# Kernel optimization log

Measured on AMD Instinct MI355X. Metric: run time of the kernel, lower is better.

## Reference

```python
import jax, jax.numpy as jnp
import numpy as np

DIM_V = 512
NUM_HEADS = 8
LN_EPS = 1e-5


def _layernorm(x):
    # LayerNorm over last dim, no affine (simplified_layer_norm=True)
    mu = jnp.mean(x, axis=-1, keepdims=True)
    var = jnp.mean(jnp.square(x - mu), axis=-1, keepdims=True)
    return (x - mu) * jax.lax.rsqrt(var + LN_EPS)


def setup_inputs() -> dict:
    key = jax.random.key(0)
    ks = jax.random.split(key, 12)
    B, Nq, Nk, dQ, dK, dV = 16, 1024, 1024, 512, 512, DIM_V
    s = 0.02
    return {
        "Q": jax.random.normal(ks[0], (B, Nq, dQ), jnp.float32),
        "K": jax.random.normal(ks[1], (B, Nk, dK), jnp.float32),
        "Wq": jax.random.normal(ks[2], (dQ, dV), jnp.float32) * s,
        "bq": jnp.zeros((dV,), jnp.float32),
        "Wk": jax.random.normal(ks[3], (dK, dV), jnp.float32) * s,
        "bk": jnp.zeros((dV,), jnp.float32),
        "Wv": jax.random.normal(ks[4], (dK, dV), jnp.float32) * s,
        "bv": jnp.zeros((dV,), jnp.float32),
        "Wo": jax.random.normal(ks[5], (dV, dV), jnp.float32) * s,
        "bo": jnp.zeros((dV,), jnp.float32),
    }


def reference(Q, K, Wq, bq, Wk, bk, Wv, bv, Wo, bo):
    H = NUM_HEADS
    dh = DIM_V // H
    q = Q @ Wq + bq            # [B, Nq, dV]
    k = K @ Wk + bk            # [B, Nk, dV]
    v = K @ Wv + bv            # [B, Nk, dV]
    B, Nq, _ = q.shape
    Nk = k.shape[1]
    qh = q.reshape(B, Nq, H, dh)
    kh = k.reshape(B, Nk, H, dh)
    vh = v.reshape(B, Nk, H, dh)
    # NOTE: faithful to source — scale by sqrt(dim_V), not sqrt(head_dim)
    scores = jnp.einsum('bqhd,bkhd->bhqk', qh, kh) / jnp.sqrt(jnp.asarray(DIM_V, q.dtype))
    A = jax.nn.softmax(scores, axis=-1)                    # [B, H, Nq, Nk]
    attn = jnp.einsum('bhqk,bkhd->bqhd', A, vh).reshape(B, Nq, DIM_V)
    O = q + attn               # residual with projected Q
    O = _layernorm(O)          # ln0 (no affine)
    O = O + jax.nn.gelu(O @ Wo + bo, approximate=False)
    O = _layernorm(O)          # ln1 (no affine)
    return O
```

## Files before the change

kernel.cpp:

```cpp
#include <hip/hip_runtime.h>
#include <hip/hip_bf16.h>
#include <math.h>

typedef __bf16 bf16;
typedef __bf16 bf16x8 __attribute__((ext_vector_type(8)));
typedef __bf16 bf16x4 __attribute__((ext_vector_type(4)));
typedef float  f32x4  __attribute__((ext_vector_type(4)));

#define MFMA16(a,b,c) __builtin_amdgcn_mfma_f32_16x16x32_bf16((a),(b),(c),0,0,0)
#define ATT_SCALE 0.0441941738241592f

__device__ __forceinline__ void async16(const bf16* g, bf16* l) {
    __builtin_amdgcn_global_load_lds((const __attribute__((address_space(1))) void*)g,
                                     (__attribute__((address_space(3))) void*)l,
                                     16, 0, 0);
}

__global__ __launch_bounds__(256) void prep_kernel(
    const float* __restrict__ Q, const float* __restrict__ K,
    const float* __restrict__ Wq, const float* __restrict__ Wk,
    const float* __restrict__ Wv, const float* __restrict__ Wo,
    bf16* __restrict__ Qb, bf16* __restrict__ Kb,
    bf16* __restrict__ WqT, bf16* __restrict__ WkT,
    bf16* __restrict__ WvT, bf16* __restrict__ WoT)
{
    __shared__ float tile[32][33];
    const int bx = blockIdx.x;
    if (bx < 8192) {
        const float* src = (bx < 4096) ? Q : K;
        bf16* dst        = (bx < 4096) ? Qb : Kb;
        int i = ((bx & 4095) * 256 + threadIdx.x) * 8;
        float4 a = *(const float4*)(src + i);
        float4 b = *(const float4*)(src + i + 4);
        bf16x8 o;
        o[0]=(bf16)a.x; o[1]=(bf16)a.y; o[2]=(bf16)a.z; o[3]=(bf16)a.w;
        o[4]=(bf16)b.x; o[5]=(bf16)b.y; o[6]=(bf16)b.z; o[7]=(bf16)b.w;
        *(bf16x8*)(dst + i) = o;
    } else {
        const int wid = bx - 8192;
        const float* W; bf16* T;
        switch (wid >> 8) {
          case 0: W=Wq; T=WqT; break;
          case 1: W=Wk; T=WkT; break;
          case 2: W=Wv; T=WvT; break;
          default: W=Wo; T=WoT; break;
        }
        const int rest = wid & 255;
        const int k0 = (rest & 15) * 32, n0 = (rest >> 4) * 32;
        const int tx = threadIdx.x & 31, ty = threadIdx.x >> 5;
        #pragma unroll
        for (int i=0;i<32;i+=8)
            tile[ty+i][tx] = W[(size_t)(k0+ty+i)*512 + n0+tx];
        __syncthreads();
        #pragma unroll
        for (int i=0;i<32;i+=8)
            T[(size_t)(n0+ty+i)*512 + k0+tx] = (bf16)tile[tx][ty+i];
    }
}

__device__ __forceinline__ void gemm_bt_body(
    const bf16* __restrict__ A, const bf16* __restrict__ BT,
    const float* __restrict__ bias,
    float* __restrict__ Cf, bf16* __restrict__ Cb, bf16* __restrict__ CvT)
{
    __shared__ bf16 As[128][32];
    __shared__ bf16 Bs[128][32];
    __shared__ bf16 Lt[64][136];
    const int m0 = blockIdx.x * 128, n0 = blockIdx.y * 128;
    const int tid = threadIdx.x;
    const int lane = tid & 63, wave = tid >> 6;
    const int qd = lane >> 4, lr = lane & 15;
    const int wm = (wave & 1) * 64, wn = (wave >> 1) * 64;

    const bf16* gA = A  + (size_t)(m0 + (tid>>2))*512 + (tid&3)*8;
    const bf16* gB = BT + (size_t)(n0 + (tid>>2))*512 + (tid&3)*8;
    bf16* lA = &As[0][0] + wave*512;
    bf16* lB = &Bs[0][0] + wave*512;

    f32x4 acc[4][4];
    #pragma unroll
    for (int i=0;i<4;i++)
      #pragma unroll
      for (int j=0;j<4;j++) acc[i][j] = (f32x4){0.f,0.f,0.f,0.f};

    for (int k0 = 0; k0 < 512; k0 += 32) {
        __syncthreads();
        async16(gA + k0,            lA);
        async16(gA + 64*512 + k0,   lA + 2048);
        async16(gB + k0,            lB);
        async16(gB + 64*512 + k0,   lB + 2048);
        __syncthreads();
        bf16x8 af[4], bfr[4];
        #pragma unroll
        for (int mi=0;mi<4;mi++) af[mi]  = *(bf16x8*)(&As[wm + mi*16 + lr][qd*8]);
        #pragma unroll
        for (int ni=0;ni<4;ni++) bfr[ni] = *(bf16x8*)(&Bs[wn + ni*16 + lr][qd*8]);
        #pragma unroll
        for (int mi=0;mi<4;mi++)
          #pragma unroll
          for (int ni=0;ni<4;ni++)
            acc[mi][ni] = MFMA16(af[mi], bfr[ni], acc[mi][ni]);
    }

    if (Cf || Cb) {
        #pragma unroll
        for (int ni=0;ni<4;ni++) {
            int n = n0 + wn + ni*16 + lr;
            float bv = bias[n];
            #pragma unroll
            for (int mi=0;mi<4;mi++) {
                int mb = m0 + wm + mi*16 + qd*4;
                #pragma unroll
                for (int r=0;r<4;r++) {
                    float v = acc[mi][ni][r] + bv;
                    if (Cf) Cf[(size_t)(mb+r)*512 + n] = v;
                    if (Cb) Cb[(size_t)(mb+r)*512 + n] = (bf16)v;
                }
            }
        }
    }
    if (CvT) {
        const int b = m0 >> 10, tok0 = m0 & 1023;
        const int row = tid >> 2, ch = tid & 3;
        #pragma unroll
        for (int half = 0; half < 2; ++half) {
            __syncthreads();
            if ((wn >> 6) == half) {
                #pragma unroll
                for (int ni=0;ni<4;ni++) {
                    int nl = ni*16 + lr;
                    float bv = bias[n0 + half*64 + nl];
                    #pragma unroll
                    for (int mi=0;mi<4;mi++)
                      #pragma unroll
                      for (int r=0;r<4;r++)
                        Lt[nl][wm + mi*16 + qd*4 + r] = (bf16)(acc[mi][ni][r] + bv);
                }
            }
            __syncthreads();
            const int h = (n0 >> 6) + half;
            uint4 x0 = *(uint4*)(&Lt[row][ch*32]);
            uint4 x1 = *(uint4*)(&Lt[row][ch*32 + 8]);
            bf16* dst = CvT + ((size_t)((b*8 + h)*64 + row))*1024 + tok0 + ch*32;
            *(uint4*)dst       = x0;
            *(uint4*)(dst + 8) = x1;
        }
    }
}

__global__ __launch_bounds__(256) void gemm_proj_kernel(
    const bf16* __restrict__ Qb, const bf16* __restrict__ Kb,
    const bf16* __restrict__ WqT, const bf16* __restrict__ WkT, const bf16* __restrict__ WvT,
    const float* __restrict__ bq, const float* __restrict__ bk, const float* __restrict__ bv,
    bf16* __restrict__ qbb, bf16* __restrict__ kbb, bf16* __restrict__ vT)
{
    switch (blockIdx.z) {
      case 0:  gemm_bt_body(Qb, WqT, bq, nullptr, qbb, nullptr); break;
      case 1:  gemm_bt_body(Kb, WkT, bk, nullptr, kbb, nullptr); break;
      default: gemm_bt_body(Kb, WvT, bv, nullptr, nullptr, vT); break;
    }
}

__global__ __launch_bounds__(256) void gemm_o_kernel(
    const bf16* __restrict__ Obf, const bf16* __restrict__ WoT,
    const float* __restrict__ bo, float* __restrict__ G32)
{
    gemm_bt_body(Obf, WoT, bo, G32, nullptr, nullptr);
}

__global__ __launch_bounds__(256, 4) void attn_kernel(
    const bf16* __restrict__ qb, const bf16* __restrict__ kb,
    const bf16* __restrict__ vT, bf16* __restrict__ attnb)
{
    const int qt = blockIdx.x, h = blockIdx.y, b = blockIdx.z;
    const int tid = threadIdx.x, lane = tid & 63, wave = tid >> 6;
    const int qd = lane >> 4, lr = lane & 15;
    const int q0 = qt*128 + wave*32;

    __shared__ bf16 Ks[64][72];
    __shared__ bf16 Vs[64][72];
    __shared__ bf16 Pl[4][32][72];

    bf16x8 aq[2][2];
    #pragma unroll
    for (int mi=0;mi<2;mi++) {
        const bf16* qrow = qb + ((size_t)(b*1024 + q0 + mi*16 + lr))*512 + h*64;
        aq[mi][0] = *(const bf16x8*)(qrow + qd*8);
        aq[mi][1] = *(const bf16x8*)(qrow + 32 + qd*8);
    }

    const int srow = tid >> 2;
    const int scol = (tid & 3) * 16;
    const bf16* kgp = kb + ((size_t)(b*1024 + srow))*512 + h*64 + scol;
    const bf16* vgp = vT + ((size_t)((b*8 + h)*64 + srow))*1024 + scol;

    uint4 k0r = *(const uint4*)(kgp);
    uint4 k1r = *(const uint4*)(kgp + 8);
    uint4 v0r = *(const uint4*)(vgp);
    uint4 v1r = *(const uint4*)(vgp + 8);

    f32x4 acc[2][4];
    #pragma unroll
    for (int mi=0;mi<2;mi++)
      #pragma unroll
      for (int ni=0;ni<4;ni++) acc[mi][ni] = (f32x4){0.f,0.f,0.f,0.f};
    float l[2][4] = {{0.f,0.f,0.f,0.f},{0.f,0.f,0.f,0.f}};

    for (int t=0; t<16; ++t) {
        __syncthreads();
        *(uint4*)(&Ks[srow][scol])   = k0r;
        *(uint4*)(&Ks[srow][scol+8]) = k1r;
        *(uint4*)(&Vs[srow][scol])   = v0r;
        *(uint4*)(&Vs[srow][scol+8]) = v1r;
        __syncthreads();
        if (t < 15) {
            const size_t ko = (size_t)(t+1)*64*512;
            const size_t vo = (size_t)(t+1)*64;
            k0r = *(const uint4*)(kgp + ko);
            k1r = *(const uint4*)(kgp + ko + 8);
            v0r = *(const uint4*)(vgp + vo);
            v1r = *(const uint4*)(vgp + vo + 8);
        }

        f32x4 s[2][4];
        #pragma unroll
        for (int mi=0;mi<2;mi++)
          #pragma unroll
          for (int ni=0;ni<4;ni++) s[mi][ni] = (f32x4){0.f,0.f,0.f,0.f};
        #pragma unroll
        for (int ni=0;ni<4;ni++) {
            bf16x8 b0 = *(bf16x8*)(&Ks[ni*16+lr][qd*8]);
            bf16x8 b1 = *(bf16x8*)(&Ks[ni*16+lr][32+qd*8]);
            #pragma unroll
            for (int mi=0;mi<2;mi++) {
                s[mi][ni] = MFMA16(aq[mi][0], b0, s[mi][ni]);
                s[mi][ni] = MFMA16(aq[mi][1], b1, s[mi][ni]);
            }
        }
        #pragma unroll
        for (int mi=0;mi<2;mi++)
          #pragma unroll
          for (int ni=0;ni<4;ni++)
            #pragma unroll
            for (int r=0;r<4;r++) {
                float pv = __expf(s[mi][ni][r] * ATT_SCALE);
                s[mi][ni][r] = pv;
                l[mi][r] += pv;
            }
        #pragma unroll
        for (int mi=0;mi<2;mi++)
          #pragma unroll
          for (int ni=0;ni<4;ni++)
            #pragma unroll
            for (int r=0;r<4;r++)
                Pl[wave][mi*16 + qd*4 + r][ni*16 + lr] = (bf16)s[mi][ni][r];
        bf16x8 ap[2][2];
        #pragma unroll
        for (int mi=0;mi<2;mi++) {
            ap[mi][0] = *(bf16x8*)(&Pl[wave][mi*16+lr][qd*8]);
            ap[mi][1] = *(bf16x8*)(&Pl[wave][mi*16+lr][32+qd*8]);
        }
        #pragma unroll
        for (int ni=0;ni<4;ni++) {
            bf16x8 v0 = *(bf16x8*)(&Vs[ni*16+lr][qd*8]);
            bf16x8 v1 = *(bf16x8*)(&Vs[ni*16+lr][32+qd*8]);
            #pragma unroll
            for (int mi=0;mi<2;mi++) {
                acc[mi][ni] = MFMA16(ap[mi][0], v0, acc[mi][ni]);
                acc[mi][ni] = MFMA16(ap[mi][1], v1, acc[mi][ni]);
            }
        }
    }

    #pragma unroll
    for (int off=1; off<16; off<<=1)
      #pragma unroll
      for (int mi=0;mi<2;mi++)
        #pragma unroll
        for (int r=0;r<4;r++) l[mi][r] += __shfl_xor(l[mi][r], off);

    #pragma unroll
    for (int mi=0;mi<2;mi++) {
        float inv[4];
        #pragma unroll
        for (int r=0;r<4;r++) inv[r] = 1.f / l[mi][r];
        #pragma unroll
        for (int ni=0;ni<4;ni++)
          #pragma unroll
          for (int r=0;r<4;r++)
            Pl[wave][qd*4+r][ni*16+lr] = (bf16)(acc[mi][ni][r] * inv[r]);
        bf16x8 oA = *(bf16x8*)(&Pl[wave][lr][qd*8]);
        bf16x8 oB = *(bf16x8*)(&Pl[wave][lr][32+qd*8]);
        bf16* dst = attnb + ((size_t)(b*1024 + q0 + mi*16 + lr))*512 + h*64;
        *(bf16x8*)(dst + qd*8)      = oA;
        *(bf16x8*)(dst + 32 + qd*8) = oB;
    }
}

__global__ __launch_bounds__(256) void ln0_kernel(
    const bf16* __restrict__ qbb, const bf16* __restrict__ attnb,
    bf16* __restrict__ Obf)
{
    const int wave = threadIdx.x >> 6, lane = threadIdx.x & 63;
    const int row = blockIdx.x*4 + wave;
    const size_t base = (size_t)row*512 + lane*8;
    bf16x8 qv = *(const bf16x8*)(qbb + base);
    bf16x8 av = *(const bf16x8*)(attnb + base);
    float x[8];
    #pragma unroll
    for (int i=0;i<8;i++) x[i] = (float)qv[i] + (float)av[i];
    float s1 = 0.f, s2 = 0.f;
    #pragma unroll
    for (int i=0;i<8;i++){ s1 += x[i]; s2 += x[i]*x[i]; }
    #pragma unroll
    for (int off=1; off<64; off<<=1) { s1 += __shfl_xor(s1, off); s2 += __shfl_xor(s2, off); }
    float mu  = s1 * (1.f/512.f);
    float var = s2 * (1.f/512.f) - mu*mu;
    float rstd = rsqrtf(var + 1e-5f);
    bf16x8 ob;
    #pragma unroll
    for (int i=0;i<8;i++) ob[i] = (bf16)((x[i]-mu)*rstd);
    *(bf16x8*)(Obf + base) = ob;
}

__global__ __launch_bounds__(256) void ln1_kernel(
    const bf16* __restrict__ Obf, const float* __restrict__ G32,
    float* __restrict__ out)
{
    const int wave = threadIdx.x >> 6, lane = threadIdx.x & 63;
    const int row = blockIdx.x*4 + wave;
    const size_t base = (size_t)row*512 + lane*8;
    bf16x8 ov = *(const bf16x8*)(Obf + base);
    float4 g0 = *(const float4*)(G32 + base);
    float4 g1 = *(const float4*)(G32 + base + 4);
    float gg[8] = {g0.x,g0.y,g0.z,g0.w,g1.x,g1.y,g1.z,g1.w};
    float x[8];
    #pragma unroll
    for (int i=0;i<8;i++) {
        float g = gg[i];
        float gelu = 0.5f * g * (1.f + erff(g * 0.70710678118654752f));
        x[i] = (float)ov[i] + gelu;
    }
    float s1 = 0.f, s2 = 0.f;
    #pragma unroll
    for (int i=0;i<8;i++){ s1 += x[i]; s2 += x[i]*x[i]; }
    #pragma unroll
    for (int off=1; off<64; off<<=1) { s1 += __shfl_xor(s1, off); s2 += __shfl_xor(s2, off); }
    float mu  = s1 * (1.f/512.f);
    float var = s2 * (1.f/512.f) - mu*mu;
    float rstd = rsqrtf(var + 1e-5f);
    float4 o0 = {(x[0]-mu)*rstd,(x[1]-mu)*rstd,(x[2]-mu)*rstd,(x[3]-mu)*rstd};
    float4 o1 = {(x[4]-mu)*rstd,(x[5]-mu)*rstd,(x[6]-mu)*rstd,(x[7]-mu)*rstd};
    *(float4*)(out + base)     = o0;
    *(float4*)(out + base + 4) = o1;
}

extern "C" void kernel_launch(void* const* d_in, const int* in_sizes, int n_in,
                              void* d_out, int out_size, void* d_ws, size_t ws_size,
                              hipStream_t stream)
{
    (void)in_sizes; (void)n_in; (void)out_size; (void)ws_size;
    const float* Q  = (const float*)d_in[0];
    const float* K  = (const float*)d_in[1];
    const float* Wq = (const float*)d_in[2];
    const float* bq = (const float*)d_in[3];
    const float* Wk = (const float*)d_in[4];
    const float* bk = (const float*)d_in[5];
    const float* Wv = (const float*)d_in[6];
    const float* bv = (const float*)d_in[7];
    const float* Wo = (const float*)d_in[8];
    const float* bo = (const float*)d_in[9];
    float* out = (float*)d_out;

    const size_t nTok = (size_t)16*1024*512;
    char* p = (char*)d_ws;
    auto alloc = [&](size_t bytes)->char* {
        char* r = p; p += (bytes + 255) & ~(size_t)255; return r;
    };
    bf16* Qb    = (bf16*)alloc(nTok*2);
    bf16* Kb    = (bf16*)alloc(nTok*2);
    bf16* WqT   = (bf16*)alloc(512*512*2);
    bf16* WkT   = (bf16*)alloc(512*512*2);
    bf16* WvT   = (bf16*)alloc(512*512*2);
    bf16* WoT   = (bf16*)alloc(512*512*2);
    bf16* qbb   = (bf16*)alloc(nTok*2);
    bf16* kbb   = (bf16*)alloc(nTok*2);
    bf16* vT    = (bf16*)alloc(nTok*2);
    bf16* attnb = (bf16*)alloc(nTok*2);
    bf16* Obf   = (bf16*)alloc(nTok*2);
    float* G32  = (float*)alloc(nTok*4);

    prep_kernel<<<9216, 256, 0, stream>>>(Q, K, Wq, Wk, Wv, Wo,
                                          Qb, Kb, WqT, WkT, WvT, WoT);
    gemm_proj_kernel<<<dim3(128,4,3), 256, 0, stream>>>(Qb, Kb, WqT, WkT, WvT,
                                                        bq, bk, bv, qbb, kbb, vT);
    attn_kernel<<<dim3(8,8,16), 256, 0, stream>>>(qbb, kbb, vT, attnb);
    ln0_kernel<<<4096, 256, 0, stream>>>(qbb, attnb, Obf);
    gemm_o_kernel<<<dim3(128,4), 256, 0, stream>>>(Obf, WoT, bo, G32);
    ln1_kernel<<<4096, 256, 0, stream>>>(Obf, G32, out);
}
```

Measured before the change: 277.2 us.

## Swizzle LDS layouts, widen GEMM K-step, fuse GELU residual into O-projection epilogue

The GEMM core now stages 64-wide K slices through XOR-swizzled shared memory, which halves the number of barrier pairs and is meant to avoid LDS bank conflicts. The attention kernel's K/V tiles and the V-transpose staging buffer drop padding in favour of an XOR swizzle, and the softmax exponent switches to exp2 with a pre-folded log2e scale. The GELU and residual add move into the O-projection epilogue, which writes a bf16 sum instead of an fp32 intermediate, so ln1 reads less memory. In exchange, the residual sum gets an extra bf16 rounding, and the epilogue does scattered per-element bf16 reads of Obf.

Result: slower. 294.9 us (+6.4%).

```diff
diff --git a/kernel.cpp b/kernel.cpp
--- a/kernel.cpp
+++ b/kernel.cpp
@@ -4,13 +4,12 @@
 
 typedef __bf16 bf16;
 typedef __bf16 bf16x8 __attribute__((ext_vector_type(8)));
-typedef __bf16 bf16x4 __attribute__((ext_vector_type(4)));
 typedef float  f32x4  __attribute__((ext_vector_type(4)));
 
 #define MFMA16(a,b,c) __builtin_amdgcn_mfma_f32_16x16x32_bf16((a),(b),(c),0,0,0)
-#define ATT_SCALE 0.0441941738241592f
-
-__device__ __forceinline__ void async16(const bf16* g, bf16* l) {
+#define ATT_SCALE_LOG2E 0.0637587160330163f
+
+__device__ __forceinline__ void async16p(const void* g, void* l) {
     __builtin_amdgcn_global_load_lds((const __attribute__((address_space(1))) void*)g,
                                      (__attribute__((address_space(3))) void*)l,
                                      16, 0, 0);
@@ -58,68 +57,97 @@
     }
 }
 
-__device__ __forceinline__ void gemm_bt_body(
+__device__ __forceinline__ void gemm_core(
     const bf16* __restrict__ A, const bf16* __restrict__ BT,
-    const float* __restrict__ bias,
-    float* __restrict__ Cf, bf16* __restrict__ Cb, bf16* __restrict__ CvT)
-{
-    __shared__ bf16 As[128][32];
-    __shared__ bf16 Bs[128][32];
-    __shared__ bf16 Lt[64][136];
+    int m0, int n0, char* smem, f32x4 (&acc)[4][4])
+{
+    bf16* As = (bf16*)smem;
+    bf16* Bs = (bf16*)(smem + 16384);
+    const int tid = threadIdx.x;
+    const int lane = tid & 63, wave = tid >> 6;
+    const int qd = lane >> 4, lr = lane & 15;
+    const int wm = (wave & 1) * 64, wn = (wave >> 1) * 64;
+
+    const int srow = tid >> 3;
+    const int sgr  = ((tid & 7) ^ (srow & 7)) * 8;
+    const bf16* gA = A  + (size_t)(m0 + srow)*512 + sgr;
+    const bf16* gB = BT + (size_t)(n0 + srow)*512 + sgr;
+    bf16* lA = As + wave*512;
+    bf16* lB = Bs + wave*512;
+
+    for (int k0 = 0; k0 < 512; k0 += 64) {
+        __syncthreads();
+        #pragma unroll
+        for (int i=0;i<4;i++) {
+            async16p(gA + k0 + (size_t)i*32*512, lA + i*2048);
+            async16p(gB + k0 + (size_t)i*32*512, lB + i*2048);
+        }
+        __syncthreads();
+        #pragma unroll
+        for (int half=0; half<2; ++half) {
+            bf16x8 af[4], bfr[4];
+            #pragma unroll
+            for (int mi=0;mi<4;mi++) {
+                int row = wm + mi*16 + lr;
+                af[mi] = *(bf16x8*)(As + row*64 + (((half*4+qd)^(lr&7))*8));
+            }
+            #pragma unroll
+            for (int ni=0;ni<4;ni++) {
+                int row = wn + ni*16 + lr;
+                bfr[ni] = *(bf16x8*)(Bs + row*64 + (((half*4+qd)^(lr&7))*8));
+            }
+            #pragma unroll
+            for (int mi=0;mi<4;mi++)
+              #pragma unroll
+              for (int ni=0;ni<4;ni++)
+                acc[mi][ni] = MFMA16(af[mi], bfr[ni], acc[mi][ni]);
+        }
+    }
+}
+
+__global__ __launch_bounds__(256, 4) void gemm_qkv_kernel(
+    const bf16* __restrict__ Qb, const bf16* __restrict__ Kb,
+    const bf16* __restrict__ WqT, const bf16* __restrict__ WkT,
+    const bf16* __restrict__ WvT,
+    const float* __restrict__ bq, const float* __restrict__ bk,
+    const float* __restrict__ bv,
+    bf16* __restrict__ qbb, bf16* __restrict__ kbb, bf16* __restrict__ vT)
+{
+    __shared__ __align__(16) char smem[32768];
+    const int z = blockIdx.z;
+    const bf16* A  = (z == 0) ? Qb  : Kb;
+    const bf16* BT = (z == 0) ? WqT : (z == 1) ? WkT : WvT;
+    const float* bb = (z == 0) ? bq : (z == 1) ? bk  : bv;
     const int m0 = blockIdx.x * 128, n0 = blockIdx.y * 128;
     const int tid = threadIdx.x;
     const int lane = tid & 63, wave = tid >> 6;
     const int qd = lane >> 4, lr = lane & 15;
     const int wm = (wave & 1) * 64, wn = (wave >> 1) * 64;
 
-    const bf16* gA = A  + (size_t)(m0 + (tid>>2))*512 + (tid&3)*8;
-    const bf16* gB = BT + (size_t)(n0 + (tid>>2))*512 + (tid&3)*8;
-    bf16* lA = &As[0][0] + wave*512;
-    bf16* lB = &Bs[0][0] + wave*512;
-
     f32x4 acc[4][4];
     #pragma unroll
     for (int i=0;i<4;i++)
       #pragma unroll
-      for (int j=0;j<4;j++) acc[i][j] = (f32x4){0.f,0.f,0.f,0.f};
-
-    for (int k0 = 0; k0 < 512; k0 += 32) {
-        __syncthreads();
-        async16(gA + k0,            lA);
-        async16(gA + 64*512 + k0,   lA + 2048);
-        async16(gB + k0,            lB);
-        async16(gB + 64*512 + k0,   lB + 2048);
-        __syncthreads();
-        bf16x8 af[4], bfr[4];
-        #pragma unroll
-        for (int mi=0;mi<4;mi++) af[mi]  = *(bf16x8*)(&As[wm + mi*16 + lr][qd*8]);
-        #pragma unroll
-        for (int ni=0;ni<4;ni++) bfr[ni] = *(bf16x8*)(&Bs[wn + ni*16 + lr][qd*8]);
-        #pragma unroll
-        for (int mi=0;mi<4;mi++)
-          #pragma unroll
-          for (int ni=0;ni<4;ni++)
-            acc[mi][ni] = MFMA16(af[mi], bfr[ni], acc[mi][ni]);
-    }
-
-    if (Cf || Cb) {
+      for (int j=0;j<4;j++) acc[i][j] = (f32x4){0,0,0,0};
+
+    gemm_core(A, BT, m0, n0, smem, acc);
+
+    if (z < 2) {
+        bf16* C = (z == 0) ? qbb : kbb;
         #pragma unroll
         for (int ni=0;ni<4;ni++) {
             int n = n0 + wn + ni*16 + lr;
-            float bv = bias[n];
+            float bv0 = bb[n];
             #pragma unroll
             for (int mi=0;mi<4;mi++) {
                 int mb = m0 + wm + mi*16 + qd*4;
                 #pragma unroll
-                for (int r=0;r<4;r++) {
-                    float v = acc[mi][ni][r] + bv;
-                    if (Cf) Cf[(size_t)(mb+r)*512 + n] = v;
-                    if (Cb) Cb[(size_t)(mb+r)*512 + n] = (bf16)v;
-                }
-            }
-        }
-    }
-    if (CvT) {
+                for (int r=0;r<4;r++)
+                    C[(size_t)(mb+r)*512 + n] = (bf16)(acc[mi][ni][r] + bv0);
+            }
+        }
+    } else {
+        bf16* Lt = (bf16*)smem;
         const int b = m0 >> 10, tok0 = m0 & 1023;
         const int row = tid >> 2, ch = tid & 3;
         #pragma unroll
@@ -129,43 +157,27 @@
                 #pragma unroll
                 for (int ni=0;ni<4;ni++) {
                     int nl = ni*16 + lr;
-                    float bv = bias[n0 + half*64 + nl];
+                    float bvv = bb[n0 + half*64 + nl];
                     #pragma unroll
                     for (int mi=0;mi<4;mi++)
                       #pragma unroll
-                      for (int r=0;r<4;r++)
-                        Lt[nl][wm + mi*16 + qd*4 + r] = (bf16)(acc[mi][ni][r] + bv);
+                      for (int r=0;r<4;r++) {
+                        int col = wm + mi*16 + qd*4 + r;
+                        Lt[nl*128 + ((((col>>3)^(nl&7))<<3) | (col&7))]
+                            = (bf16)(acc[mi][ni][r] + bvv);
+                      }
                 }
             }
             __syncthreads();
             const int h = (n0 >> 6) + half;
-            uint4 x0 = *(uint4*)(&Lt[row][ch*32]);
-            uint4 x1 = *(uint4*)(&Lt[row][ch*32 + 8]);
-            bf16* dst = CvT + ((size_t)((b*8 + h)*64 + row))*1024 + tok0 + ch*32;
-            *(uint4*)dst       = x0;
-            *(uint4*)(dst + 8) = x1;
-        }
-    }
-}
-
-__global__ __launch_bounds__(256) void gemm_proj_kernel(
-    const bf16* __restrict__ Qb, const bf16* __restrict__ Kb,
-    const bf16* __restrict__ WqT, const bf16* __restrict__ WkT, const bf16* __restrict__ WvT,
-    const float* __restrict__ bq, const float* __restrict__ bk, const float* __restrict__ bv,
-    bf16* __restrict__ qbb, bf16* __restrict__ kbb, bf16* __restrict__ vT)
-{
-    switch (blockIdx.z) {
-      case 0:  gemm_bt_body(Qb, WqT, bq, nullptr, qbb, nullptr); break;
-      case 1:  gemm_bt_body(Kb, WkT, bk, nullptr, kbb, nullptr); break;
-      default: gemm_bt_body(Kb, WvT, bv, nullptr, nullptr, vT); break;
-    }
-}
-
-__global__ __launch_bounds__(256) void gemm_o_kernel(
-    const bf16* __restrict__ Obf, const bf16* __restrict__ WoT,
-    const float* __restrict__ bo, float* __restrict__ G32)
-{
-    gemm_bt_body(Obf, WoT, bo, G32, nullptr, nullptr);
+            bf16* dst = vT + ((size_t)((b*8 + h)*64 + row))*1024 + tok0 + ch*32;
+            #pragma unroll
+            for (int s=0;s<4;s++) {
+                int g = (ch*4 + s) ^ (row & 7);
+                *(uint4*)(dst + s*8) = *(uint4*)(Lt + row*128 + g*8);
+            }
+        }
+    }
 }
 
 __global__ __launch_bounds__(256, 4) void attn_kernel(
@@ -177,8 +189,8 @@
     const int qd = lane >> 4, lr = lane & 15;
     const int q0 = qt*128 + wave*32;
 
-    __shared__ bf16 Ks[64][72];
-    __shared__ bf16 Vs[64][72];
+    __shared__ bf16 Ks[64*64];
+    __shared__ bf16 Vs[64*64];
     __shared__ bf16 Pl[4][32][72];
 
     bf16x8 aq[2][2];
@@ -190,9 +202,11 @@
     }
 
     const int srow = tid >> 2;
-    const int scol = (tid & 3) * 16;
-    const bf16* kgp = kb + ((size_t)(b*1024 + srow))*512 + h*64 + scol;
-    const bf16* vgp = vT + ((size_t)((b*8 + h)*64 + srow))*1024 + scol;
+    const int c2 = (tid & 3) * 2;
+    const int wg0 = ((c2  ) ^ (srow & 7)) * 8;
+    const int wg1 = ((c2+1) ^ (srow & 7)) * 8;
+    const bf16* kgp = kb + ((size_t)(b*1024 + srow))*512 + h*64 + c2*8;
+    const bf16* vgp = vT + ((size_t)((b*8 + h)*64 + srow))*1024 + c2*8;
 
     uint4 k0r = *(const uint4*)(kgp);
     uint4 k1r = *(const uint4*)(kgp + 8);
@@ -203,34 +217,34 @@
     #pragma unroll
     for (int mi=0;mi<2;mi++)
       #pragma unroll
-      for (int ni=0;ni<4;ni++) acc[mi][ni] = (f32x4){0.f,0.f,0.f,0.f};
-    float l[2][4] = {{0.f,0.f,0.f,0.f},{0.f,0.f,0.f,0.f}};
+      for (int ni=0;ni<4;ni++) acc[mi][ni] = (f32x4){0,0,0,0};
+    float l[2][4] = {{0,0,0,0},{0,0,0,0}};
 
     for (int t=0; t<16; ++t) {
         __syncthreads();
-        *(uint4*)(&Ks[srow][scol])   = k0r;
-        *(uint4*)(&Ks[srow][scol+8]) = k1r;
-        *(uint4*)(&Vs[srow][scol])   = v0r;
-        *(uint4*)(&Vs[srow][scol+8]) = v1r;
+        *(uint4*)(&Ks[srow*64 + wg0]) = k0r;
+        *(uint4*)(&Ks[srow*64 + wg1]) = k1r;
+        *(uint4*)(&Vs[srow*64 + wg0]) = v0r;
+        *(uint4*)(&Vs[srow*64 + wg1]) = v1r;
         __syncthreads();
         if (t < 15) {
-            const size_t ko = (size_t)(t+1)*64*512;
-            const size_t vo = (size_t)(t+1)*64;
-            k0r = *(const uint4*)(kgp + ko);
-            k1r = *(const uint4*)(kgp + ko + 8);
-            v0r = *(const uint4*)(vgp + vo);
-            v1r = *(const uint4*)(vgp + vo + 8);
+            const size_t kk = (size_t)(t+1)*64;
+            k0r = *(const uint4*)(kgp + kk*512);
+            k1r = *(const uint4*)(kgp + kk*512 + 8);
+            v0r = *(const uint4*)(vgp + kk);
+            v1r = *(const uint4*)(vgp + kk + 8);
         }
 
         f32x4 s[2][4];
         #pragma unroll
         for (int mi=0;mi<2;mi++)
           #pragma unroll
-          for (int ni=0;ni<4;ni++) s[mi][ni] = (f32x4){0.f,0.f,0.f,0.f};
+          for (int ni=0;ni<4;ni++) s[mi][ni] = (f32x4){0,0,0,0};
         #pragma unroll
         for (int ni=0;ni<4;ni++) {
-            bf16x8 b0 = *(bf16x8*)(&Ks[ni*16+lr][qd*8]);
-            bf16x8 b1 = *(bf16x8*)(&Ks[ni*16+lr][32+qd*8]);
+            int row = ni*16 + lr;
+            bf16x8 b0 = *(bf16x8*)(Ks + row*64 + (((qd  )^(lr&7))*8));
+            bf16x8 b1 = *(bf16x8*)(Ks + row*64 + (((qd+4)^(lr&7))*8));
             #pragma unroll
             for (int mi=0;mi<2;mi++) {
                 s[mi][ni] = MFMA16(aq[mi][0], b0, s[mi][ni]);
@@ -243,7 +257,7 @@
           for (int ni=0;ni<4;ni++)
             #pragma unroll
             for (int r=0;r<4;r++) {
-                float pv = __expf(s[mi][ni][r] * ATT_SCALE);
+                float pv = exp2f(s[mi][ni][r] * ATT_SCALE_LOG2E);
                 s[mi][ni][r] = pv;
                 l[mi][r] += pv;
             }
@@ -262,8 +276,9 @@
         }
         #pragma unroll
         for (int ni=0;ni<4;ni++) {
-            bf16x8 v0 = *(bf16x8*)(&Vs[ni*16+lr][qd*8]);
-            bf16x8 v1 = *(bf16x8*)(&Vs[ni*16+lr][32+qd*8]);
+            int row = ni*16 + lr;
+            bf16x8 v0 = *(bf16x8*)(Vs + row*64 + (((qd  )^(lr&7))*8));
+            bf16x8 v1 = *(bf16x8*)(Vs + row*64 + (((qd+4)^(lr&7))*8));
             #pragma unroll
             for (int mi=0;mi<2;mi++) {
                 acc[mi][ni] = MFMA16(ap[mi][0], v0, acc[mi][ni]);
@@ -323,24 +338,53 @@
     *(bf16x8*)(Obf + base) = ob;
 }
 
+__global__ __launch_bounds__(256, 4) void gemm_o_kernel(
+    const bf16* __restrict__ Obf, const bf16* __restrict__ WoT,
+    const float* __restrict__ bo, bf16* __restrict__ xb)
+{
+    __shared__ __align__(16) char smem[32768];
+    const int m0 = blockIdx.x * 128, n0 = blockIdx.y * 128;
+    const int tid = threadIdx.x;
+    const int lane = tid & 63, wave = tid >> 6;
+    const int qd = lane >> 4, lr = lane & 15;
+    const int wm = (wave & 1) * 64, wn = (wave >> 1) * 64;
+
+    f32x4 acc[4][4];
+    #pragma unroll
+    for (int i=0;i<4;i++)
+      #pragma unroll
+      for (int j=0;j<4;j++) acc[i][j] = (f32x4){0,0,0,0};
+
+    gemm_core(Obf, WoT, m0, n0, smem, acc);
+
+    #pragma unroll
+    for (int ni=0;ni<4;ni++) {
+        int n = n0 + wn + ni*16 + lr;
+        float bv = bo[n];
+        #pragma unroll
+        for (int mi=0;mi<4;mi++) {
+            int mb = m0 + wm + mi*16 + qd*4;
+            #pragma unroll
+            for (int r=0;r<4;r++) {
+                float g = acc[mi][ni][r] + bv;
+                float gelu = 0.5f * g * (1.f + erff(g * 0.70710678118654752f));
+                size_t idx = (size_t)(mb+r)*512 + n;
+                xb[idx] = (bf16)((float)Obf[idx] + gelu);
+            }
+        }
+    }
+}
+
 __global__ __launch_bounds__(256) void ln1_kernel(
-    const bf16* __restrict__ Obf, const float* __restrict__ G32,
-    float* __restrict__ out)
+    const bf16* __restrict__ xb, float* __restrict__ out)
 {
     const int wave = threadIdx.x >> 6, lane = threadIdx.x & 63;
     const int row = blockIdx.x*4 + wave;
     const size_t base = (size_t)row*512 + lane*8;
-    bf16x8 ov = *(const bf16x8*)(Obf + base);
-    float4 g0 = *(const float4*)(G32 + base);
-    float4 g1 = *(const float4*)(G32 + base + 4);
-    float gg[8] = {g0.x,g0.y,g0.z,g0.w,g1.x,g1.y,g1.z,g1.w};
+    bf16x8 xv = *(const bf16x8*)(xb + base);
     float x[8];
     #pragma unroll
-    for (int i=0;i<8;i++) {
-        float g = gg[i];
-        float gelu = 0.5f * g * (1.f + erff(g * 0.70710678118654752f));
-        x[i] = (float)ov[i] + gelu;
-    }
+    for (int i=0;i<8;i++) x[i] = (float)xv[i];
     float s1 = 0.f, s2 = 0.f;
     #pragma unroll
     for (int i=0;i<8;i++){ s1 += x[i]; s2 += x[i]*x[i]; }
@@ -388,14 +432,14 @@
     bf16* vT    = (bf16*)alloc(nTok*2);
     bf16* attnb = (bf16*)alloc(nTok*2);
     bf16* Obf   = (bf16*)alloc(nTok*2);
-    float* G32  = (float*)alloc(nTok*4);
+    bf16* xb    = (bf16*)alloc(nTok*2);
 
     prep_kernel<<<9216, 256, 0, stream>>>(Q, K, Wq, Wk, Wv, Wo,
                                           Qb, Kb, WqT, WkT, WvT, WoT);
-    gemm_proj_kernel<<<dim3(128,4,3), 256, 0, stream>>>(Qb, Kb, WqT, WkT, WvT,
-                                                        bq, bk, bv, qbb, kbb, vT);
+    gemm_qkv_kernel<<<dim3(128,4,3), 256, 0, stream>>>(Qb, Kb, WqT, WkT, WvT,
+                                                       bq, bk, bv, qbb, kbb, vT);
     attn_kernel<<<dim3(8,8,16), 256, 0, stream>>>(qbb, kbb, vT, attnb);
     ln0_kernel<<<4096, 256, 0, stream>>>(qbb, attnb, Obf);
-    gemm_o_kernel<<<dim3(128,4), 256, 0, stream>>>(Obf, WoT, bo, G32);
-    ln1_kernel<<<4096, 256, 0, stream>>>(Obf, G32, out);
-}
+    gemm_o_kernel<<<dim3(128,4), 256, 0, stream>>>(Obf, WoT, bo, xb);
+    ln1_kernel<<<4096, 256, 0, stream>>>(xb, out);
+}
```
